# Kernel tuning notes

Hardware: AMD Instinct MI355X
Metric: run time of the kernel (lower is better)

## Reference

```python
import jax, jax.numpy as jnp
import numpy as np

POOL = 3      # pooling_size
EPS = 0.006   # constant added to each segment mean in the original code


def setup_inputs() -> dict:
    key = jax.random.key(0)
    k1, k2 = jax.random.split(key)
    B, N, D = 8, 3072, 1024          # N divisible by POOL -> no remainder branch
    steps = N // POOL
    x = jax.random.normal(k1, (B, N, D), dtype=jnp.float32)
    # (start, end) shot boundaries, sorted so start <= end, values in [0, N)
    graph = jnp.sort(jax.random.randint(k2, (B, steps, 2), 0, N, dtype=jnp.int64), axis=-1)
    return {"x": x, "graph": graph}


def reference(x, graph):
    B, N, D = x.shape
    steps = N // POOL
    # Exclusive+inclusive prefix sums: c[b, k] = sum over x[b, :k]  -> [B, N+1, D]
    c = jnp.concatenate([jnp.zeros((B, 1, D), x.dtype), jnp.cumsum(x, axis=1)], axis=1)
    s = graph[..., 0]                # [B, steps]
    e = graph[..., 1]                # [B, steps]
    idx_e = jnp.broadcast_to((e + 1)[..., None], (B, steps, D))
    idx_s = jnp.broadcast_to(s[..., None], (B, steps, D))
    seg_sum = jnp.take_along_axis(c, idx_e, axis=1) - jnp.take_along_axis(c, idx_s, axis=1)
    seg_len = (e - s + 1).astype(x.dtype)[..., None]
    seg_mean = seg_sum / seg_len + EPS            # [B, steps, D]
    # fixed-size window mean over consecutive POOL frames
    win_mean = x.reshape(B, steps, POOL, D).mean(axis=2)   # [B, steps, D]
    # original appends (segment mean, window mean) per step -> interleave
    out = jnp.stack([seg_mean, win_mean], axis=2).reshape(B, 2 * steps, D)
    return out
```

## Files before the change

### kernel.cpp

```cpp
#include <hip/hip_runtime.h>


constexpr int Bdim  = 8;
constexpr int Nn    = 3072;
constexpr int Dd    = 1024;
constexpr int STEPS = 1024;
constexpr int CHW   = 8;
constexpr int CHR   = 24;
constexpr int NCH   = 128;
constexpr int KT    = 4;
constexpr int NKT   = 256;
constexpr int D4    = Dd / 4;
constexpr float EPS = 0.006f;

constexpr size_t R_E = (size_t)Bdim * Nn * Dd;
constexpr size_t P_E = (size_t)Bdim * NCH * Dd;

typedef float nat_f4 __attribute__((ext_vector_type(4)));

__device__ __forceinline__ float4 f4add(float4 a, float4 b) {
    return make_float4(a.x + b.x, a.y + b.y, a.z + b.z, a.w + b.w);
}

__device__ __forceinline__ float4 f4sel(bool c, float4 a, float4 b) {
    return make_float4(c ? a.x : b.x, c ? a.y : b.y,
                       c ? a.z : b.z, c ? a.w : b.w);
}

__device__ __forceinline__ void nt_store(float4 v, float4* p) {
    nat_f4 nv = {v.x, v.y, v.z, v.w};
    __builtin_nontemporal_store(nv, reinterpret_cast<nat_f4*>(p));
}

__device__ __forceinline__ float4 nt_load(const float4* p) {
    nat_f4 nv = __builtin_nontemporal_load(reinterpret_cast<const nat_f4*>(p));
    return make_float4(nv.x, nv.y, nv.z, nv.w);
}

__global__ __launch_bounds__(256)
void k1_scan(const float4* __restrict__ x4, float4* __restrict__ out4,
             float4* __restrict__ R4, float4* __restrict__ P4) {
    const int t  = threadIdx.x;
    const int ch = blockIdx.x;
    const int b  = blockIdx.y;
    const int k0 = ch * CHW;
    const int r0 = ch * CHR;

    const float4* xp = x4   + ((size_t)(b * Nn + r0)) * D4 + t;
    float4*       rl = R4   + ((size_t)(b * Nn + r0)) * D4 + t;
    float4*       op = out4 + ((size_t)b * 2 * STEPS) * D4 + t;

    float4 v[CHR];
#pragma unroll
    for (int i = 0; i < CHR; ++i)
        v[i] = nt_load(&xp[(size_t)i * D4]);

#pragma unroll
    for (int wi = 0; wi < CHW; ++wi) {
        float4 w = f4add(f4add(v[3 * wi], v[3 * wi + 1]), v[3 * wi + 2]);
        float4 wm = make_float4(w.x * (1.f / 3.f), w.y * (1.f / 3.f),
                                w.z * (1.f / 3.f), w.w * (1.f / 3.f));
        nt_store(wm, &op[(size_t)(2 * (k0 + wi) + 1) * D4]);
    }

    float4 run = make_float4(0.f, 0.f, 0.f, 0.f);
#pragma unroll
    for (int i = 0; i < CHR; ++i) {
        rl[(size_t)i * D4] = run;
        run = f4add(run, v[i]);
    }
    P4[((size_t)b * NCH + ch) * D4 + t] = run;
}

__global__ __launch_bounds__(256)
void k2_chscan(const float4* __restrict__ P4, float4* __restrict__ O4) {
    __shared__ float4 part[8][33];
    const int cw  = threadIdx.x & 31;
    const int seg = threadIdx.x >> 5;
    const int col = blockIdx.x * 32 + cw;
    const int b   = blockIdx.y;

    const float4* p = P4 + (size_t)b * NCH * D4 + col;
    float4 v[16];
    float4 sum = make_float4(0.f, 0.f, 0.f, 0.f);
#pragma unroll
    for (int i = 0; i < 16; ++i) {
        v[i] = p[(size_t)(seg * 16 + i) * D4];
        sum = f4add(sum, v[i]);
    }
    part[seg][cw] = sum;
    __syncthreads();
    if (threadIdx.x < 32) {
        float4 run = make_float4(0.f, 0.f, 0.f, 0.f);
#pragma unroll
        for (int s = 0; s < 8; ++s) {
            float4 t2 = part[s][threadIdx.x];
            part[s][threadIdx.x] = run;
            run = f4add(run, t2);
        }
    }
    __syncthreads();
    float4 run = part[seg][cw];
    float4* o = O4 + (size_t)b * (NCH + 1) * D4 + col;
#pragma unroll
    for (int i = 0; i < 16; ++i) {
        o[(size_t)(seg * 16 + i) * D4] = run;
        run = f4add(run, v[i]);
    }
    if (seg == 7) o[(size_t)NCH * D4] = run;
}

__global__ __launch_bounds__(256)
void k3_gather(const float4* __restrict__ R4, const float4* __restrict__ O4,
               const int* __restrict__ graph, float4* __restrict__ out4) {
    const int t  = threadIdx.x;
    const int kt = blockIdx.x;
    const int b  = blockIdx.y;

    const int* gp = graph + ((size_t)(b * STEPS + kt * KT)) * 2;
    const int4 ga = *reinterpret_cast<const int4*>(gp);
    const int4 gb = *reinterpret_cast<const int4*>(gp + 4);
    const int sA[KT] = {ga.x, ga.z, gb.x, gb.z};
    const int eA[KT] = {ga.y, ga.w, gb.y, gb.w};

    const float4* rb = R4  + (size_t)b * Nn * D4 + t;
    const float4* oc = O4  + (size_t)b * (NCH + 1) * D4 + t;
    float4*       ob = out4 + (size_t)b * 2 * STEPS * D4 + t;

    float4 o1[KT], r1[KT], o2[KT], r2[KT];
    int ieA[KT];
#pragma unroll
    for (int u = 0; u < KT; ++u) {
        int s  = sA[u];
        int c1 = s / CHR;
        o1[u] = oc[(size_t)c1 * D4];
        r1[u] = rb[(size_t)s * D4];

        int ie = eA[u] + 1;      ieA[u] = ie;
        int c2 = ie / CHR;
        o2[u] = oc[(size_t)c2 * D4];
        int rc = ie < Nn ? ie : Nn - 1;
        r2[u] = rb[(size_t)rc * D4];
    }

    const float4 z4 = make_float4(0.f, 0.f, 0.f, 0.f);
#pragma unroll
    for (int u = 0; u < KT; ++u) {
        float4 cs = f4add(o1[u], r1[u]);
        float4 ce = f4add(o2[u], f4sel(ieA[u] < Nn, r2[u], z4));

        float inv = 1.f / (float)(eA[u] - sA[u] + 1);
        float4 res = make_float4((ce.x - cs.x) * inv + EPS,
                                 (ce.y - cs.y) * inv + EPS,
                                 (ce.z - cs.z) * inv + EPS,
                                 (ce.w - cs.w) * inv + EPS);
        int k = kt * KT + u;
        nt_store(res, &ob[(size_t)(2 * k) * D4]);
    }
}

extern "C" void kernel_launch(void* const* d_in, const int* in_sizes, int n_in,
                              void* d_out, int out_size, void* d_ws, size_t ws_size,
                              hipStream_t stream) {
    const float* x     = (const float*)d_in[0];
    const int*   graph = (const int*)d_in[1];
    float*       out   = (float*)d_out;

    float* R = (float*)d_ws;
    float* P = R + R_E;
    float* O = P + P_E;

    dim3 g1(NCH, Bdim);
    k1_scan<<<g1, 256, 0, stream>>>((const float4*)x, (float4*)out,
                                    (float4*)R, (float4*)P);
    dim3 g2(D4 / 32, Bdim);
    k2_chscan<<<g2, 256, 0, stream>>>((const float4*)P, (float4*)O);
    dim3 g3(NKT, Bdim);
    k3_gather<<<g3, 256, 0, stream>>>((const float4*)R, (const float4*)O,
                                      graph, (float4*)out);
}
```

Measured before the change: 195.0 us.

## Fuse scan, chunk-scan and gather into one cooperative kernel with grid syncs

Merges the three kernels into a single cooperative launch of 512 blocks. Each block scans two chunks, then 64 blocks do the cross-chunk prefix scan, then every block gathers 16 segments, with grid-wide syncs between the phases. This removes two kernel launch boundaries and their idle gaps. In exchange it adds grid-sync overhead, leaves most blocks idle during the middle phase, and gives each phase fewer, larger blocks, which lowers parallelism and memory-level overlap.

Measured after the change: 347.6 us. 78.3% more time.

```diff
diff --git a/kernel.cpp b/kernel.cpp
--- a/kernel.cpp
+++ b/kernel.cpp
@@ -1,4 +1,7 @@
 #include <hip/hip_runtime.h>
+#include <hip/hip_cooperative_groups.h>
+
+namespace cg = cooperative_groups;
 
 
 constexpr int Bdim  = 8;
@@ -8,8 +11,6 @@
 constexpr int CHW   = 8;
 constexpr int CHR   = 24;
 constexpr int NCH   = 128;
-constexpr int KT    = 4;
-constexpr int NKT   = 256;
 constexpr int D4    = Dd / 4;
 constexpr float EPS = 0.006f;
 
@@ -37,125 +38,121 @@
     return make_float4(nv.x, nv.y, nv.z, nv.w);
 }
 
-__global__ __launch_bounds__(256)
-void k1_scan(const float4* __restrict__ x4, float4* __restrict__ out4,
-             float4* __restrict__ R4, float4* __restrict__ P4) {
+__global__ __launch_bounds__(256, 2)
+void fused(const float4* __restrict__ x4, const int* __restrict__ graph,
+           float4* __restrict__ out4, float4* __restrict__ R4,
+           float4* __restrict__ P4, float4* __restrict__ O4) {
     const int t  = threadIdx.x;
-    const int ch = blockIdx.x;
+    const int bx = blockIdx.x;
     const int b  = blockIdx.y;
-    const int k0 = ch * CHW;
-    const int r0 = ch * CHR;
+    const float4 z4 = make_float4(0.f, 0.f, 0.f, 0.f);
 
-    const float4* xp = x4   + ((size_t)(b * Nn + r0)) * D4 + t;
-    float4*       rl = R4   + ((size_t)(b * Nn + r0)) * D4 + t;
-    float4*       op = out4 + ((size_t)b * 2 * STEPS) * D4 + t;
+    float4* opb = out4 + ((size_t)b * 2 * STEPS) * D4 + t;
+#pragma unroll
+    for (int cc = 0; cc < 2; ++cc) {
+        const int ch = bx * 2 + cc;
+        const int k0 = ch * CHW;
+        const int r0 = ch * CHR;
+        const float4* xp = x4 + ((size_t)(b * Nn + r0)) * D4 + t;
+        float4*       rl = R4 + ((size_t)(b * Nn + r0)) * D4 + t;
 
-    float4 v[CHR];
+        float4 v[CHR];
 #pragma unroll
-    for (int i = 0; i < CHR; ++i)
-        v[i] = nt_load(&xp[(size_t)i * D4]);
+        for (int i = 0; i < CHR; ++i)
+            v[i] = nt_load(&xp[(size_t)i * D4]);
 
 #pragma unroll
-    for (int wi = 0; wi < CHW; ++wi) {
-        float4 w = f4add(f4add(v[3 * wi], v[3 * wi + 1]), v[3 * wi + 2]);
-        float4 wm = make_float4(w.x * (1.f / 3.f), w.y * (1.f / 3.f),
-                                w.z * (1.f / 3.f), w.w * (1.f / 3.f));
-        nt_store(wm, &op[(size_t)(2 * (k0 + wi) + 1) * D4]);
+        for (int wi = 0; wi < CHW; ++wi) {
+            float4 w = f4add(f4add(v[3 * wi], v[3 * wi + 1]), v[3 * wi + 2]);
+            float4 wm = make_float4(w.x * (1.f / 3.f), w.y * (1.f / 3.f),
+                                    w.z * (1.f / 3.f), w.w * (1.f / 3.f));
+            nt_store(wm, &opb[(size_t)(2 * (k0 + wi) + 1) * D4]);
+        }
+
+        float4 run = z4;
+#pragma unroll
+        for (int i = 0; i < CHR; ++i) {
+            rl[(size_t)i * D4] = run;
+            run = f4add(run, v[i]);
+        }
+        P4[((size_t)b * NCH + ch) * D4 + t] = run;
     }
 
-    float4 run = make_float4(0.f, 0.f, 0.f, 0.f);
+    cg::this_grid().sync();
+
+    __shared__ float4 part[8][33];
+    if (bx < 8) {
+        const int cw  = t & 31;
+        const int seg = t >> 5;
+        const int col = bx * 32 + cw;
+
+        const float4* p = P4 + (size_t)b * NCH * D4 + col;
+        float4 v2[16];
+        float4 sum = z4;
 #pragma unroll
-    for (int i = 0; i < CHR; ++i) {
-        rl[(size_t)i * D4] = run;
-        run = f4add(run, v[i]);
-    }
-    P4[((size_t)b * NCH + ch) * D4 + t] = run;
-}
-
-__global__ __launch_bounds__(256)
-void k2_chscan(const float4* __restrict__ P4, float4* __restrict__ O4) {
-    __shared__ float4 part[8][33];
-    const int cw  = threadIdx.x & 31;
-    const int seg = threadIdx.x >> 5;
-    const int col = blockIdx.x * 32 + cw;
-    const int b   = blockIdx.y;
-
-    const float4* p = P4 + (size_t)b * NCH * D4 + col;
-    float4 v[16];
-    float4 sum = make_float4(0.f, 0.f, 0.f, 0.f);
+        for (int i = 0; i < 16; ++i) {
+            v2[i] = p[(size_t)(seg * 16 + i) * D4];
+            sum = f4add(sum, v2[i]);
+        }
+        part[seg][cw] = sum;
+        __syncthreads();
+        if (t < 32) {
+            float4 run = z4;
 #pragma unroll
-    for (int i = 0; i < 16; ++i) {
-        v[i] = p[(size_t)(seg * 16 + i) * D4];
-        sum = f4add(sum, v[i]);
-    }
-    part[seg][cw] = sum;
-    __syncthreads();
-    if (threadIdx.x < 32) {
-        float4 run = make_float4(0.f, 0.f, 0.f, 0.f);
+            for (int s = 0; s < 8; ++s) {
+                float4 t2 = part[s][t];
+                part[s][t] = run;
+                run = f4add(run, t2);
+            }
+        }
+        __syncthreads();
+        float4 run = part[seg][cw];
+        float4* o = O4 + (size_t)b * (NCH + 1) * D4 + col;
 #pragma unroll
-        for (int s = 0; s < 8; ++s) {
-            float4 t2 = part[s][threadIdx.x];
-            part[s][threadIdx.x] = run;
-            run = f4add(run, t2);
+        for (int i = 0; i < 16; ++i) {
+            o[(size_t)(seg * 16 + i) * D4] = run;
+            run = f4add(run, v2[i]);
         }
-    }
-    __syncthreads();
-    float4 run = part[seg][cw];
-    float4* o = O4 + (size_t)b * (NCH + 1) * D4 + col;
-#pragma unroll
-    for (int i = 0; i < 16; ++i) {
-        o[(size_t)(seg * 16 + i) * D4] = run;
-        run = f4add(run, v[i]);
-    }
-    if (seg == 7) o[(size_t)NCH * D4] = run;
-}
-
-__global__ __launch_bounds__(256)
-void k3_gather(const float4* __restrict__ R4, const float4* __restrict__ O4,
-               const int* __restrict__ graph, float4* __restrict__ out4) {
-    const int t  = threadIdx.x;
-    const int kt = blockIdx.x;
-    const int b  = blockIdx.y;
-
-    const int* gp = graph + ((size_t)(b * STEPS + kt * KT)) * 2;
-    const int4 ga = *reinterpret_cast<const int4*>(gp);
-    const int4 gb = *reinterpret_cast<const int4*>(gp + 4);
-    const int sA[KT] = {ga.x, ga.z, gb.x, gb.z};
-    const int eA[KT] = {ga.y, ga.w, gb.y, gb.w};
-
-    const float4* rb = R4  + (size_t)b * Nn * D4 + t;
-    const float4* oc = O4  + (size_t)b * (NCH + 1) * D4 + t;
-    float4*       ob = out4 + (size_t)b * 2 * STEPS * D4 + t;
-
-    float4 o1[KT], r1[KT], o2[KT], r2[KT];
-    int ieA[KT];
-#pragma unroll
-    for (int u = 0; u < KT; ++u) {
-        int s  = sA[u];
-        int c1 = s / CHR;
-        o1[u] = oc[(size_t)c1 * D4];
-        r1[u] = rb[(size_t)s * D4];
-
-        int ie = eA[u] + 1;      ieA[u] = ie;
-        int c2 = ie / CHR;
-        o2[u] = oc[(size_t)c2 * D4];
-        int rc = ie < Nn ? ie : Nn - 1;
-        r2[u] = rb[(size_t)rc * D4];
+        if (seg == 7) o[(size_t)NCH * D4] = run;
     }
 
-    const float4 z4 = make_float4(0.f, 0.f, 0.f, 0.f);
+    cg::this_grid().sync();
+
+    const float4* rb = R4 + (size_t)b * Nn * D4 + t;
+    const float4* oc = O4 + (size_t)b * (NCH + 1) * D4 + t;
+    for (int g = 0; g < 4; ++g) {
+        const int kbase = bx * 16 + g * 4;
+        const int* gp = graph + ((size_t)(b * STEPS + kbase)) * 2;
+        const int4 ga = *reinterpret_cast<const int4*>(gp);
+        const int4 gb2 = *reinterpret_cast<const int4*>(gp + 4);
+        const int sA[4] = {ga.x, ga.z, gb2.x, gb2.z};
+        const int eA[4] = {ga.y, ga.w, gb2.y, gb2.w};
+
+        float4 o1[4], r1[4], o2[4], r2[4];
+        int ieA[4];
 #pragma unroll
-    for (int u = 0; u < KT; ++u) {
-        float4 cs = f4add(o1[u], r1[u]);
-        float4 ce = f4add(o2[u], f4sel(ieA[u] < Nn, r2[u], z4));
+        for (int u = 0; u < 4; ++u) {
+            int s  = sA[u];
+            o1[u] = oc[(size_t)(s / CHR) * D4];
+            r1[u] = rb[(size_t)s * D4];
 
-        float inv = 1.f / (float)(eA[u] - sA[u] + 1);
-        float4 res = make_float4((ce.x - cs.x) * inv + EPS,
-                                 (ce.y - cs.y) * inv + EPS,
-                                 (ce.z - cs.z) * inv + EPS,
-                                 (ce.w - cs.w) * inv + EPS);
-        int k = kt * KT + u;
-        nt_store(res, &ob[(size_t)(2 * k) * D4]);
+            int ie = eA[u] + 1;      ieA[u] = ie;
+            o2[u] = oc[(size_t)(ie / CHR) * D4];
+            int rc = ie < Nn ? ie : Nn - 1;
+            r2[u] = rb[(size_t)rc * D4];
+        }
+#pragma unroll
+        for (int u = 0; u < 4; ++u) {
+            float4 cs = f4add(o1[u], r1[u]);
+            float4 ce = f4add(o2[u], f4sel(ieA[u] < Nn, r2[u], z4));
+
+            float inv = 1.f / (float)(eA[u] - sA[u] + 1);
+            float4 res = make_float4((ce.x - cs.x) * inv + EPS,
+                                     (ce.y - cs.y) * inv + EPS,
+                                     (ce.z - cs.z) * inv + EPS,
+                                     (ce.w - cs.w) * inv + EPS);
+            nt_store(res, &opb[(size_t)(2 * (kbase + u)) * D4]);
+        }
     }
 }
 
@@ -170,12 +167,14 @@
     float* P = R + R_E;
     float* O = P + P_E;
 
-    dim3 g1(NCH, Bdim);
-    k1_scan<<<g1, 256, 0, stream>>>((const float4*)x, (float4*)out,
-                                    (float4*)R, (float4*)P);
-    dim3 g2(D4 / 32, Bdim);
-    k2_chscan<<<g2, 256, 0, stream>>>((const float4*)P, (float4*)O);
-    dim3 g3(NKT, Bdim);
-    k3_gather<<<g3, 256, 0, stream>>>((const float4*)R, (const float4*)O,
-                                      graph, (float4*)out);
+    const float4* x4   = (const float4*)x;
+    float4*       out4 = (float4*)out;
+    float4*       R4   = (float4*)R;
+    float4*       P4   = (float4*)P;
+    float4*       O4   = (float4*)O;
+
+    void* args[] = {(void*)&x4, (void*)&graph, (void*)&out4,
+                    (void*)&R4, (void*)&P4, (void*)&O4};
+    hipLaunchCooperativeKernel((const void*)fused, dim3(64, Bdim), dim3(256),
+                               args, 0, stream);
 }
```

## Scatter prefix values only to rows referenced by segment boundaries

Applied to the files above, without the earlier changes.

Adds a small bucketing kernel that records, for each frame row, which output steps need its local prefix value (up to a fixed cap per row). The scan kernel then writes prefix values only to those step slots in a compact per-step buffer, instead of storing the full local prefix for every frame. The combine kernel then reads that buffer sequentially rather than gathering rows at random. This cuts intermediate write traffic and improves read locality. The cost is an extra launch, atomic-based bucketing, and any events beyond the per-row cap are silently dropped.

Result: no change. 193.2 us (-0.9%).

```diff
diff --git a/kernel.cpp b/kernel.cpp
--- a/kernel.cpp
+++ b/kernel.cpp
@@ -11,10 +11,12 @@
 constexpr int KT    = 4;
 constexpr int NKT   = 256;
 constexpr int D4    = Dd / 4;
+constexpr int RCAP  = 12;
 constexpr float EPS = 0.006f;
 
-constexpr size_t R_E = (size_t)Bdim * Nn * Dd;
+constexpr size_t T_E = (size_t)Bdim * 2 * STEPS * Dd;
 constexpr size_t P_E = (size_t)Bdim * NCH * Dd;
+constexpr size_t O_E = (size_t)Bdim * (NCH + 1) * Dd;
 
 typedef float nat_f4 __attribute__((ext_vector_type(4)));
 
@@ -38,17 +40,47 @@
 }
 
 __global__ __launch_bounds__(256)
+void k0_bucket(const int* __restrict__ graph, int* __restrict__ rowcnt,
+               int* __restrict__ evrow) {
+    const int b = blockIdx.x;
+    __shared__ int cnt[Nn];
+    for (int i = threadIdx.x; i < Nn; i += 256) cnt[i] = 0;
+    __syncthreads();
+    for (int k = threadIdx.x; k < STEPS; k += 256) {
+        const int2 se = *reinterpret_cast<const int2*>(
+            graph + ((size_t)(b * STEPS + k)) * 2);
+        const int s  = se.x;
+        const int ie = se.y + 1;
+        int sl = atomicAdd(&cnt[s], 1);
+        if (sl < RCAP)
+            evrow[((size_t)b * Nn + s) * RCAP + sl] = 2 * k;
+        if (ie < Nn) {
+            int sl2 = atomicAdd(&cnt[ie], 1);
+            if (sl2 < RCAP)
+                evrow[((size_t)b * Nn + ie) * RCAP + sl2] = 2 * k + 1;
+        }
+    }
+    __syncthreads();
+    for (int i = threadIdx.x; i < Nn; i += 256)
+        rowcnt[(size_t)b * Nn + i] = min(cnt[i], RCAP);
+}
+
+__global__ __launch_bounds__(256)
 void k1_scan(const float4* __restrict__ x4, float4* __restrict__ out4,
-             float4* __restrict__ R4, float4* __restrict__ P4) {
+             float4* __restrict__ T4, float4* __restrict__ P4,
+             const int* __restrict__ rowcnt, const int* __restrict__ evrow) {
     const int t  = threadIdx.x;
     const int ch = blockIdx.x;
     const int b  = blockIdx.y;
     const int k0 = ch * CHW;
     const int r0 = ch * CHR;
+    const float4 z4 = make_float4(0.f, 0.f, 0.f, 0.f);
 
     const float4* xp = x4   + ((size_t)(b * Nn + r0)) * D4 + t;
-    float4*       rl = R4   + ((size_t)(b * Nn + r0)) * D4 + t;
     float4*       op = out4 + ((size_t)b * 2 * STEPS) * D4 + t;
+    float4*       Tb = T4   + ((size_t)b * 2 * STEPS) * D4 + t;
+    const int*    rc = rowcnt + (size_t)b * Nn + r0;
+    const int*    ev = evrow + ((size_t)b * Nn + r0) * RCAP;
 
     float4 v[CHR];
 #pragma unroll
@@ -63,11 +95,15 @@
         nt_store(wm, &op[(size_t)(2 * (k0 + wi) + 1) * D4]);
     }
 
-    float4 run = make_float4(0.f, 0.f, 0.f, 0.f);
-#pragma unroll
-    for (int i = 0; i < CHR; ++i) {
-        rl[(size_t)i * D4] = run;
-        run = f4add(run, v[i]);
+    float4 run = z4;
+#pragma unroll
+    for (int j = 0; j < CHR; ++j) {
+        const int nj = rc[j];
+        for (int q = 0; q < nj; ++q) {
+            const int trow = ev[j * RCAP + q];
+            Tb[(size_t)trow * D4] = run;
+        }
+        run = f4add(run, v[j]);
     }
     P4[((size_t)b * NCH + ch) * D4 + t] = run;
 }
@@ -111,8 +147,8 @@
 }
 
 __global__ __launch_bounds__(256)
-void k3_gather(const float4* __restrict__ R4, const float4* __restrict__ O4,
-               const int* __restrict__ graph, float4* __restrict__ out4) {
+void k4_combine(const float4* __restrict__ T4, const float4* __restrict__ O4,
+                const int* __restrict__ graph, float4* __restrict__ out4) {
     const int t  = threadIdx.x;
     const int kt = blockIdx.x;
     const int b  = blockIdx.y;
@@ -123,38 +159,36 @@
     const int sA[KT] = {ga.x, ga.z, gb.x, gb.z};
     const int eA[KT] = {ga.y, ga.w, gb.y, gb.w};
 
-    const float4* rb = R4  + (size_t)b * Nn * D4 + t;
-    const float4* oc = O4  + (size_t)b * (NCH + 1) * D4 + t;
+    const float4* Tb = T4 + (size_t)b * 2 * STEPS * D4 + t;
+    const float4* oc = O4 + (size_t)b * (NCH + 1) * D4 + t;
     float4*       ob = out4 + (size_t)b * 2 * STEPS * D4 + t;
 
-    float4 o1[KT], r1[KT], o2[KT], r2[KT];
+    float4 ts[KT], te[KT], o1[KT], o2[KT];
     int ieA[KT];
+    const float4 tot = oc[(size_t)NCH * D4];
 #pragma unroll
     for (int u = 0; u < KT; ++u) {
-        int s  = sA[u];
-        int c1 = s / CHR;
-        o1[u] = oc[(size_t)c1 * D4];
-        r1[u] = rb[(size_t)s * D4];
-
-        int ie = eA[u] + 1;      ieA[u] = ie;
-        int c2 = ie / CHR;
+        const int k = kt * KT + u;
+        ts[u] = Tb[(size_t)(2 * k) * D4];
+        te[u] = Tb[(size_t)(2 * k + 1) * D4];
+        const int s = sA[u];
+        const int ie = eA[u] + 1;  ieA[u] = ie;
+        o1[u] = oc[(size_t)(s / CHR) * D4];
+        const int c2 = ie < Nn ? ie / CHR : 0;
         o2[u] = oc[(size_t)c2 * D4];
-        int rc = ie < Nn ? ie : Nn - 1;
-        r2[u] = rb[(size_t)rc * D4];
-    }
-
-    const float4 z4 = make_float4(0.f, 0.f, 0.f, 0.f);
+    }
+
 #pragma unroll
     for (int u = 0; u < KT; ++u) {
-        float4 cs = f4add(o1[u], r1[u]);
-        float4 ce = f4add(o2[u], f4sel(ieA[u] < Nn, r2[u], z4));
+        float4 cs = f4add(o1[u], ts[u]);
+        float4 ce = f4sel(ieA[u] < Nn, f4add(o2[u], te[u]), tot);
 
         float inv = 1.f / (float)(eA[u] - sA[u] + 1);
         float4 res = make_float4((ce.x - cs.x) * inv + EPS,
                                  (ce.y - cs.y) * inv + EPS,
                                  (ce.z - cs.z) * inv + EPS,
                                  (ce.w - cs.w) * inv + EPS);
-        int k = kt * KT + u;
+        const int k = kt * KT + u;
         nt_store(res, &ob[(size_t)(2 * k) * D4]);
     }
 }
@@ -166,16 +200,19 @@
     const int*   graph = (const int*)d_in[1];
     float*       out   = (float*)d_out;
 
-    float* R = (float*)d_ws;
-    float* P = R + R_E;
+    float* T = (float*)d_ws;
+    float* P = T + T_E;
     float* O = P + P_E;
-
+    int*   rowcnt = (int*)(O + O_E);
+    int*   evrow  = rowcnt + (size_t)Bdim * Nn;
+
+    k0_bucket<<<dim3(Bdim), 256, 0, stream>>>(graph, rowcnt, evrow);
     dim3 g1(NCH, Bdim);
     k1_scan<<<g1, 256, 0, stream>>>((const float4*)x, (float4*)out,
-                                    (float4*)R, (float4*)P);
+                                    (float4*)T, (float4*)P, rowcnt, evrow);
     dim3 g2(D4 / 32, Bdim);
     k2_chscan<<<g2, 256, 0, stream>>>((const float4*)P, (float4*)O);
-    dim3 g3(NKT, Bdim);
-    k3_gather<<<g3, 256, 0, stream>>>((const float4*)R, (const float4*)O,
-                                      graph, (float4*)out);
-}
+    dim3 g4(NKT, Bdim);
+    k4_combine<<<g4, 256, 0, stream>>>((const float4*)T, (const float4*)O,
+                                       graph, (float4*)out);
+}
```

## Fuse chunk scan with decoupled lookback and scatter only needed prefix rows

Applied to the files above, without the earlier changes.

Replaces the three-kernel scheme with one scan kernel plus a combine step. The scan kernel takes an ordered ticket per chunk, publishes chunk totals with flags, and waits on earlier chunks to get its running offset. Each block builds a shared-memory list of which graph boundaries fall in its chunk and writes prefix values only for those rows into a compact buffer of 2*STEPS rows. This drops the full N-row prefix buffer and the separate chunk-scan kernel, cutting global writes. In exchange it adds spin-wait serialisation across blocks, a lookback that reads a number of partial sums growing with chunk index, and a fixed cap of 16 boundaries per row that silently drops any beyond it.

Result: slower. 456.9 us (+134.3%).

```diff
diff --git a/kernel.cpp b/kernel.cpp
--- a/kernel.cpp
+++ b/kernel.cpp
@@ -11,20 +11,16 @@
 constexpr int KT    = 4;
 constexpr int NKT   = 256;
 constexpr int D4    = Dd / 4;
+constexpr int RCAP  = 16;
 constexpr float EPS = 0.006f;
 
-constexpr size_t R_E = (size_t)Bdim * Nn * Dd;
+constexpr size_t T_E = (size_t)Bdim * 2 * STEPS * Dd;
 constexpr size_t P_E = (size_t)Bdim * NCH * Dd;
 
 typedef float nat_f4 __attribute__((ext_vector_type(4)));
 
 __device__ __forceinline__ float4 f4add(float4 a, float4 b) {
     return make_float4(a.x + b.x, a.y + b.y, a.z + b.z, a.w + b.w);
-}
-
-__device__ __forceinline__ float4 f4sel(bool c, float4 a, float4 b) {
-    return make_float4(c ? a.x : b.x, c ? a.y : b.y,
-                       c ? a.z : b.z, c ? a.w : b.w);
 }
 
 __device__ __forceinline__ void nt_store(float4 v, float4* p) {
@@ -38,23 +34,66 @@
 }
 
 __global__ __launch_bounds__(256)
-void k1_scan(const float4* __restrict__ x4, float4* __restrict__ out4,
-             float4* __restrict__ R4, float4* __restrict__ P4) {
-    const int t  = threadIdx.x;
-    const int ch = blockIdx.x;
-    const int b  = blockIdx.y;
-    const int k0 = ch * CHW;
-    const int r0 = ch * CHR;
+void k0_zero(int* __restrict__ flags, int* __restrict__ tick) {
+    const int t = threadIdx.x;
+    for (int i = t; i < Bdim * NCH; i += 256) flags[i] = 0;
+    if (t < Bdim) tick[t] = 0;
+}
 
-    const float4* xp = x4   + ((size_t)(b * Nn + r0)) * D4 + t;
-    float4*       rl = R4   + ((size_t)(b * Nn + r0)) * D4 + t;
-    float4*       op = out4 + ((size_t)b * 2 * STEPS) * D4 + t;
+__global__ __launch_bounds__(256)
+void k1_scan(const float4* __restrict__ x4, const int* __restrict__ graph,
+             float4* __restrict__ out4, float4* __restrict__ T4,
+             float4* __restrict__ P4, int* __restrict__ flags,
+             int* __restrict__ tick) {
+    const int t = threadIdx.x;
+    const int b = blockIdx.y;
+    const float4 z4 = make_float4(0.f, 0.f, 0.f, 0.f);
 
+    __shared__ int s_tk;
+    if (t == 0) s_tk = atomicAdd(&tick[b], 1);
+    __syncthreads();
+    const int tk = s_tk;
+    const int r0 = tk * CHR;
+    const int k0 = tk * CHW;
+
+    __shared__ int cnt[CHR + 1];
+    __shared__ int lst[CHR + 1][RCAP];
+    for (int i = t; i < CHR + 1; i += 256) cnt[i] = 0;
+    __syncthreads();
+    for (int k = t; k < STEPS; k += 256) {
+        const int2 se = *reinterpret_cast<const int2*>(
+            graph + ((size_t)(b * STEPS + k)) * 2);
+        const int js = se.x - r0;
+        if (js >= 0 && js < CHR) {
+            int p = atomicAdd(&cnt[js], 1);
+            if (p < RCAP) lst[js][p] = 2 * k;
+        }
+        const int je = se.y + 1 - r0;
+        if (je >= 0 && (je < CHR || (je == CHR && tk == NCH - 1))) {
+            int p = atomicAdd(&cnt[je], 1);
+            if (p < RCAP) lst[je][p] = 2 * k + 1;
+        }
+    }
+    __syncthreads();
+
+    const float4* xp = x4 + ((size_t)(b * Nn + r0)) * D4 + t;
     float4 v[CHR];
 #pragma unroll
     for (int i = 0; i < CHR; ++i)
         v[i] = nt_load(&xp[(size_t)i * D4]);
 
+    float4 tot = z4;
+#pragma unroll
+    for (int i = 0; i < CHR; ++i) tot = f4add(tot, v[i]);
+
+    P4[((size_t)b * NCH + tk) * D4 + t] = tot;
+    __threadfence();
+    __syncthreads();
+    if (t == 0)
+        __hip_atomic_store(&flags[b * NCH + tk], 1,
+                           __ATOMIC_RELEASE, __HIP_MEMORY_SCOPE_AGENT);
+
+    float4* op = out4 + ((size_t)b * 2 * STEPS) * D4 + t;
 #pragma unroll
     for (int wi = 0; wi < CHW; ++wi) {
         float4 w = f4add(f4add(v[3 * wi], v[3 * wi + 1]), v[3 * wi + 2]);
@@ -63,56 +102,38 @@
         nt_store(wm, &op[(size_t)(2 * (k0 + wi) + 1) * D4]);
     }
 
-    float4 run = make_float4(0.f, 0.f, 0.f, 0.f);
+    if (t < tk) {
+        const int* fp = &flags[b * NCH + t];
+        while (__hip_atomic_load(fp, __ATOMIC_ACQUIRE,
+                                 __HIP_MEMORY_SCOPE_AGENT) == 0)
+            __builtin_amdgcn_s_sleep(2);
+    }
+    __syncthreads();
+
+    float4 off = z4;
+    const float4* pb = P4 + (size_t)b * NCH * D4 + t;
+    for (int i = 0; i < tk; ++i)
+        off = f4add(off, pb[(size_t)i * D4]);
+
+    float4* Tb = T4 + ((size_t)b * 2 * STEPS) * D4 + t;
+    float4 run = off;
 #pragma unroll
-    for (int i = 0; i < CHR; ++i) {
-        rl[(size_t)i * D4] = run;
-        run = f4add(run, v[i]);
+    for (int j = 0; j < CHR; ++j) {
+        const int nj = min(cnt[j], RCAP);
+        for (int q = 0; q < nj; ++q)
+            Tb[(size_t)lst[j][q] * D4] = run;
+        run = f4add(run, v[j]);
     }
-    P4[((size_t)b * NCH + ch) * D4 + t] = run;
+    if (tk == NCH - 1) {
+        const int nj = min(cnt[CHR], RCAP);
+        for (int q = 0; q < nj; ++q)
+            Tb[(size_t)lst[CHR][q] * D4] = run;
+    }
 }
 
 __global__ __launch_bounds__(256)
-void k2_chscan(const float4* __restrict__ P4, float4* __restrict__ O4) {
-    __shared__ float4 part[8][33];
-    const int cw  = threadIdx.x & 31;
-    const int seg = threadIdx.x >> 5;
-    const int col = blockIdx.x * 32 + cw;
-    const int b   = blockIdx.y;
-
-    const float4* p = P4 + (size_t)b * NCH * D4 + col;
-    float4 v[16];
-    float4 sum = make_float4(0.f, 0.f, 0.f, 0.f);
-#pragma unroll
-    for (int i = 0; i < 16; ++i) {
-        v[i] = p[(size_t)(seg * 16 + i) * D4];
-        sum = f4add(sum, v[i]);
-    }
-    part[seg][cw] = sum;
-    __syncthreads();
-    if (threadIdx.x < 32) {
-        float4 run = make_float4(0.f, 0.f, 0.f, 0.f);
-#pragma unroll
-        for (int s = 0; s < 8; ++s) {
-            float4 t2 = part[s][threadIdx.x];
-            part[s][threadIdx.x] = run;
-            run = f4add(run, t2);
-        }
-    }
-    __syncthreads();
-    float4 run = part[seg][cw];
-    float4* o = O4 + (size_t)b * (NCH + 1) * D4 + col;
-#pragma unroll
-    for (int i = 0; i < 16; ++i) {
-        o[(size_t)(seg * 16 + i) * D4] = run;
-        run = f4add(run, v[i]);
-    }
-    if (seg == 7) o[(size_t)NCH * D4] = run;
-}
-
-__global__ __launch_bounds__(256)
-void k3_gather(const float4* __restrict__ R4, const float4* __restrict__ O4,
-               const int* __restrict__ graph, float4* __restrict__ out4) {
+void k4_combine(const float4* __restrict__ T4, const int* __restrict__ graph,
+                float4* __restrict__ out4) {
     const int t  = threadIdx.x;
     const int kt = blockIdx.x;
     const int b  = blockIdx.y;
@@ -123,38 +144,25 @@
     const int sA[KT] = {ga.x, ga.z, gb.x, gb.z};
     const int eA[KT] = {ga.y, ga.w, gb.y, gb.w};
 
-    const float4* rb = R4  + (size_t)b * Nn * D4 + t;
-    const float4* oc = O4  + (size_t)b * (NCH + 1) * D4 + t;
+    const float4* Tb = T4 + (size_t)b * 2 * STEPS * D4 + t;
     float4*       ob = out4 + (size_t)b * 2 * STEPS * D4 + t;
 
-    float4 o1[KT], r1[KT], o2[KT], r2[KT];
-    int ieA[KT];
+    float4 ts[KT], te[KT];
 #pragma unroll
     for (int u = 0; u < KT; ++u) {
-        int s  = sA[u];
-        int c1 = s / CHR;
-        o1[u] = oc[(size_t)c1 * D4];
-        r1[u] = rb[(size_t)s * D4];
-
-        int ie = eA[u] + 1;      ieA[u] = ie;
-        int c2 = ie / CHR;
-        o2[u] = oc[(size_t)c2 * D4];
-        int rc = ie < Nn ? ie : Nn - 1;
-        r2[u] = rb[(size_t)rc * D4];
+        const int k = kt * KT + u;
+        ts[u] = Tb[(size_t)(2 * k) * D4];
+        te[u] = Tb[(size_t)(2 * k + 1) * D4];
     }
 
-    const float4 z4 = make_float4(0.f, 0.f, 0.f, 0.f);
 #pragma unroll
     for (int u = 0; u < KT; ++u) {
-        float4 cs = f4add(o1[u], r1[u]);
-        float4 ce = f4add(o2[u], f4sel(ieA[u] < Nn, r2[u], z4));
-
-        float inv = 1.f / (float)(eA[u] - sA[u] + 1);
-        float4 res = make_float4((ce.x - cs.x) * inv + EPS,
-                                 (ce.y - cs.y) * inv + EPS,
-                                 (ce.z - cs.z) * inv + EPS,
-                                 (ce.w - cs.w) * inv + EPS);
-        int k = kt * KT + u;
+        const float inv = 1.f / (float)(eA[u] - sA[u] + 1);
+        float4 res = make_float4((te[u].x - ts[u].x) * inv + EPS,
+                                 (te[u].y - ts[u].y) * inv + EPS,
+                                 (te[u].z - ts[u].z) * inv + EPS,
+                                 (te[u].w - ts[u].w) * inv + EPS);
+        const int k = kt * KT + u;
         nt_store(res, &ob[(size_t)(2 * k) * D4]);
     }
 }
@@ -166,16 +174,15 @@
     const int*   graph = (const int*)d_in[1];
     float*       out   = (float*)d_out;
 
-    float* R = (float*)d_ws;
-    float* P = R + R_E;
-    float* O = P + P_E;
+    float* T = (float*)d_ws;
+    float* P = T + T_E;
+    int*   flags = (int*)(P + P_E);
+    int*   tick  = flags + (size_t)Bdim * NCH;
 
+    k0_zero<<<dim3(1), 256, 0, stream>>>(flags, tick);
     dim3 g1(NCH, Bdim);
-    k1_scan<<<g1, 256, 0, stream>>>((const float4*)x, (float4*)out,
-                                    (float4*)R, (float4*)P);
-    dim3 g2(D4 / 32, Bdim);
-    k2_chscan<<<g2, 256, 0, stream>>>((const float4*)P, (float4*)O);
-    dim3 g3(NKT, Bdim);
-    k3_gather<<<g3, 256, 0, stream>>>((const float4*)R, (const float4*)O,
-                                      graph, (float4*)out);
+    k1_scan<<<g1, 256, 0, stream>>>((const float4*)x, graph, (float4*)out,
+                                    (float4*)T, (float4*)P, flags, tick);
+    dim3 g4(NKT, Bdim);
+    k4_combine<<<g4, 256, 0, stream>>>((const float4*)T, graph, (float4*)out);
 }
```
